# Optimization experiments

Hardware: AMD Instinct MI355X
Metric: run time of the kernel (lower is better)

The kernel has to match this reference:

```python
import jax, jax.numpy as jnp
import numpy as np

D_MODEL = 1024
N_HEADS = 16
D_K = 64


def setup_inputs() -> dict:
    key = jax.random.key(0)
    ks = jax.random.split(key, 9)
    dkh = D_K * N_HEADS
    s = 1.0 / np.sqrt(D_MODEL)
    so = 1.0 / np.sqrt(dkh)
    return {
        "x": jax.random.normal(ks[0], (2, 2048, D_MODEL), dtype=jnp.float32),
        "Wq": jax.random.normal(ks[1], (D_MODEL, dkh), dtype=jnp.float32) * s,
        "bq": jnp.zeros((dkh,), dtype=jnp.float32),
        "Wk": jax.random.normal(ks[2], (D_MODEL, dkh), dtype=jnp.float32) * s,
        "bk": jnp.zeros((dkh,), dtype=jnp.float32),
        "Wv": jax.random.normal(ks[3], (D_MODEL, dkh), dtype=jnp.float32) * s,
        "bv": jnp.zeros((dkh,), dtype=jnp.float32),
        "Wo": jax.random.normal(ks[4], (dkh, D_MODEL), dtype=jnp.float32) * so,
        "bo": jnp.zeros((D_MODEL,), dtype=jnp.float32),
    }


def reference(x, Wq, bq, Wk, bk, Wv, bv, Wo, bo):
    B, S, _ = x.shape
    # project and split heads: [B, S, H, Dk] -> [B, H, S, Dk]
    def split(t):
        return t.reshape(B, S, N_HEADS, D_K).transpose(0, 2, 1, 3)
    q = split(x @ Wq + bq)
    k = split(x @ Wk + bk)
    v = split(x @ Wv + bv)
    scores = jnp.einsum("bhsd,bhtd->bhst", q, k) / jnp.sqrt(jnp.float32(D_K))
    weights = jax.nn.softmax(scores, axis=-1)
    out = jnp.einsum("bhst,bhtd->bhsd", weights, v)  # [B, H, S, Dk]
    out = out.transpose(0, 2, 1, 3).reshape(B, S, N_HEADS * D_K)
    return out @ Wo + bo
```

## Files before the change

### kernel.cpp

```cpp
#include <hip/hip_runtime.h>

typedef unsigned short u16;
typedef unsigned int u32;
typedef short bf16x4 __attribute__((ext_vector_type(4)));
typedef short bf16x8 __attribute__((ext_vector_type(8)));
typedef float f32x4 __attribute__((ext_vector_type(4)));
typedef u32 u32x2 __attribute__((ext_vector_type(2)));
typedef u32 u32x4 __attribute__((ext_vector_type(4)));

#define DEVINL __device__ __forceinline__

DEVINL u16 f2bf(float f) {
    u32 u = __builtin_bit_cast(u32, f);
    u32 r = u + 0x7fffu + ((u >> 16) & 1u);
    return (u16)(r >> 16);
}

DEVINL u32 pack2(float a, float b) {
    return (u32)f2bf(a) | ((u32)f2bf(b) << 16);
}

__global__ __launch_bounds__(256) void cast_x_kernel(const float4* __restrict__ in,
                                                     u16* __restrict__ outp) {
    int i = blockIdx.x * 256 + threadIdx.x;
    float4 v = in[i];
    ushort4 o;
    o.x = f2bf(v.x); o.y = f2bf(v.y); o.z = f2bf(v.z); o.w = f2bf(v.w);
    *(ushort4*)&outp[(size_t)i * 4] = o;
}

__global__ __launch_bounds__(256) void transpose_cast(
    const float* __restrict__ W0, const float* __restrict__ W1,
    const float* __restrict__ W2, const float* __restrict__ W3,
    u16* __restrict__ T0, u16* __restrict__ T1,
    u16* __restrict__ T2, u16* __restrict__ T3) {
    __shared__ __align__(16) u16 lds[64 * 68];
    int bid = blockIdx.x;
    const float* W; u16* T;
    switch (bid >> 8) {
        case 0:  W = W0; T = T0; break;
        case 1:  W = W1; T = T1; break;
        case 2:  W = W2; T = T2; break;
        default: W = W3; T = T3; break;
    }
    int tile = bid & 255;
    int k0 = (tile >> 4) << 6;
    int n0 = (tile & 15) << 6;
    int t = threadIdx.x;
    int rk = t >> 2;
    int cb = (t & 3) << 4;
#pragma unroll
    for (int j = 0; j < 4; ++j) {
        float4 v = *(const float4*)&W[(size_t)(k0 + rk) * 1024 + n0 + cb + 4 * j];
        ushort4 o;
        o.x = f2bf(v.x); o.y = f2bf(v.y); o.z = f2bf(v.z); o.w = f2bf(v.w);
        *(ushort4*)&lds[rk * 68 + cb + 4 * j] = o;
    }
    __syncthreads();
    int rn = t >> 2;
#pragma unroll
    for (int j2 = 0; j2 < 2; ++j2) {
        u16 tmp[8];
#pragma unroll
        for (int u = 0; u < 8; ++u)
            tmp[u] = lds[(cb + 8 * j2 + u) * 68 + rn];
        *(uint4*)&T[(size_t)(n0 + rn) * 1024 + k0 + cb + 8 * j2] = *(uint4*)tmp;
    }
}

template <int MODE>
__global__ __launch_bounds__(256) void gemm_kernel(
    const u16* __restrict__ A,
    const u16* __restrict__ W0t, const u16* __restrict__ W1t, const u16* __restrict__ W2t,
    const float* __restrict__ b0, const float* __restrict__ b1, const float* __restrict__ b2,
    u16* __restrict__ Oq, u16* __restrict__ Ok, u16* __restrict__ Ov,
    float* __restrict__ Fout) {
    constexpr int NB = (MODE == 0) ? 24 : 8;
    const int mb = blockIdx.x / NB, nb = blockIdx.x % NB;
    const int m0 = mb * 128, n0 = nb * 128;
    const int tid = threadIdx.x, lane = tid & 63, w = tid >> 6;
    const int wr = w >> 1, wc = w & 1;
    const int c = lane & 15, g = lane >> 4;

    __shared__ __align__(16) u16 Alds[128 * 64];
    __shared__ __align__(16) u16 Blds[128 * 64];

    const u16* Wt; const float* bias; int ncol0;
    if (MODE == 0) {
        const int tsel = n0 >> 10;
        Wt   = (tsel == 0) ? W0t : ((tsel == 1) ? W1t : W2t);
        bias = (tsel == 0) ? b0  : ((tsel == 1) ? b1  : b2);
        ncol0 = n0 & 1023;
    } else {
        Wt = W0t; bias = b0; ncol0 = n0;
    }

    const u16* Asrc = A  + (size_t)(m0    + 32 * w + (lane >> 3)) * 1024 + (lane & 7) * 8;
    const u16* Bsrc = Wt + (size_t)(ncol0 + 32 * w + (lane >> 3)) * 1024 + (lane & 7) * 8;
    u16* AldsW = &Alds[(32 * w) * 64];
    u16* BldsW = &Blds[(32 * w) * 64];

    f32x4 acc[4][4] = {};

    for (int kt = 0; kt < 16; ++kt) {
        const int k0 = kt * 64;
#pragma unroll
        for (int i = 0; i < 4; ++i) {
            __builtin_amdgcn_global_load_lds(
                (const __attribute__((address_space(1))) void*)(Asrc + k0 + i * 8 * 1024),
                (__attribute__((address_space(3))) void*)(AldsW + i * 8 * 64), 16, 0, 0);
            __builtin_amdgcn_global_load_lds(
                (const __attribute__((address_space(1))) void*)(Bsrc + k0 + i * 8 * 1024),
                (__attribute__((address_space(3))) void*)(BldsW + i * 8 * 64), 16, 0, 0);
        }
        __syncthreads();
#pragma unroll
        for (int kk = 0; kk < 2; ++kk) {
            bf16x8 af[4], bfr[4];
#pragma unroll
            for (int mf = 0; mf < 4; ++mf)
                af[mf] = *(const bf16x8*)&Alds[(c + 16 * mf + 64 * wr) * 64 + 8 * g + 32 * kk];
#pragma unroll
            for (int nf = 0; nf < 4; ++nf)
                bfr[nf] = *(const bf16x8*)&Blds[(c + 16 * nf + 64 * wc) * 64 + 8 * g + 32 * kk];
#pragma unroll
            for (int mf = 0; mf < 4; ++mf)
#pragma unroll
                for (int nf = 0; nf < 4; ++nf)
                    acc[mf][nf] = __builtin_amdgcn_mfma_f32_16x16x32_bf16(
                        af[mf], bfr[nf], acc[mf][nf], 0, 0, 0);
        }
        __syncthreads();
    }

    float biasv[4];
#pragma unroll
    for (int nf = 0; nf < 4; ++nf) biasv[nf] = bias[ncol0 + 64 * wc + 16 * nf + c];

    if (MODE == 0) {
        const int bi = m0 >> 11;
        const int tsel = n0 >> 10;
        if (tsel < 2) {
            u16* Odst = (tsel == 0) ? Oq : Ok;
            const float sc = (tsel == 0) ? 0.125f : 1.0f;
#pragma unroll
            for (int nf = 0; nf < 4; ++nf) {
                const int n_in = ncol0 + 64 * wc + 16 * nf + c;
                const int h = n_in >> 6, d = n_in & 63;
                u16* base = Odst + ((size_t)(bi * 16 + h)) * 2048 * 64 + d;
#pragma unroll
                for (int mf = 0; mf < 4; ++mf)
#pragma unroll
                    for (int r = 0; r < 4; ++r) {
                        const int m = m0 + 64 * wr + 16 * mf + 4 * g + r;
                        const int s = m & 2047;
                        base[(size_t)s * 64] = f2bf((acc[mf][nf][r] + biasv[nf]) * sc);
                    }
            }
        } else {
#pragma unroll
            for (int nf = 0; nf < 4; ++nf) {
                const int n_in = ncol0 + 64 * wc + 16 * nf + c;
                const int h = n_in >> 6, d = n_in & 63;
                u16* base = Ov + ((size_t)((bi * 16 + h) * 64 + d)) * 2048;
#pragma unroll
                for (int mf = 0; mf < 4; ++mf) {
                    const int s = (m0 & 2047) + 64 * wr + 16 * mf + 4 * g;
                    u32x2 pr = {pack2(acc[mf][nf][0] + biasv[nf], acc[mf][nf][1] + biasv[nf]),
                                pack2(acc[mf][nf][2] + biasv[nf], acc[mf][nf][3] + biasv[nf])};
                    *(u32x2*)&base[s] = pr;
                }
            }
        }
    } else {
#pragma unroll
        for (int mf = 0; mf < 4; ++mf)
#pragma unroll
            for (int r = 0; r < 4; ++r) {
                const int m = m0 + 64 * wr + 16 * mf + 4 * g + r;
                float* rowp = Fout + (size_t)m * 1024 + n0 + 64 * wc;
#pragma unroll
                for (int nf = 0; nf < 4; ++nf)
                    rowp[16 * nf + c] = acc[mf][nf][r] + biasv[nf];
            }
    }
}

__global__ __launch_bounds__(256) void attn_kernel(
    const u16* __restrict__ Q, const u16* __restrict__ K, const u16* __restrict__ Vt,
    u16* __restrict__ O) {
    const int bid0 = blockIdx.x;
    const int bid = (bid0 & 7) * 128 + (bid0 >> 3);
    const int qb = bid & 31, h = (bid >> 5) & 15, b = bid >> 9;
    const int tid = threadIdx.x, lane = tid & 63, w = tid >> 6;
    const int c = lane & 15, g = lane >> 4;

    __shared__ __align__(16) u16 Klds[2][64 * 72];
    __shared__ __align__(16) u16 Vlds[2][64 * 72];

    const size_t hoff = ((size_t)(b * 16 + h)) * 2048 * 64;
    const u16* Qh = Q + hoff;
    const u16* Kh = K + hoff;
    const u16* Vh = Vt + hoff;

    const int q = qb * 64 + w * 16 + c;
    bf16x8 qf[2];
#pragma unroll
    for (int kk = 0; kk < 2; ++kk)
        qf[kk] = *(const bf16x8*)&Qh[(size_t)q * 64 + 8 * g + 32 * kk];

    f32x4 oacc[4] = {};
    float mrun = -3.0e38f, lrun = 0.f;

    const int srow = tid >> 3;
    const int scol = (tid & 7) * 8;

    {
        uint4 ka  = *(const uint4*)&Kh[(size_t)srow * 64 + scol];
        uint4 kb2 = *(const uint4*)&Kh[(size_t)(srow + 32) * 64 + scol];
        uint4 va  = *(const uint4*)&Vh[(size_t)srow * 2048 + scol];
        uint4 vb  = *(const uint4*)&Vh[(size_t)(srow + 32) * 2048 + scol];
        *(uint4*)&Klds[0][srow * 72 + scol] = ka;
        *(uint4*)&Klds[0][(srow + 32) * 72 + scol] = kb2;
        *(uint4*)&Vlds[0][srow * 72 + scol] = va;
        *(uint4*)&Vlds[0][(srow + 32) * 72 + scol] = vb;
    }
    __syncthreads();

    for (int kt = 0; kt < 32; ++kt) {
        const int cur = kt & 1, nxt = cur ^ 1;
        uint4 ka, kb2, va, vb;
        if (kt < 31) {
            ka  = *(const uint4*)&Kh[(size_t)((kt + 1) * 64 + srow) * 64 + scol];
            kb2 = *(const uint4*)&Kh[(size_t)((kt + 1) * 64 + srow + 32) * 64 + scol];
            va  = *(const uint4*)&Vh[(size_t)srow * 2048 + (kt + 1) * 64 + scol];
            vb  = *(const uint4*)&Vh[(size_t)(srow + 32) * 2048 + (kt + 1) * 64 + scol];
        }
        const u16* Kb0 = &Klds[cur][0];
        const u16* Vb0 = &Vlds[cur][0];

        f32x4 sacc[4] = {};
#pragma unroll
        for (int T = 0; T < 4; ++T)
#pragma unroll
            for (int kk = 0; kk < 2; ++kk) {
                bf16x8 kf = *(const bf16x8*)&Kb0[(16 * T + c) * 72 + 8 * g + 32 * kk];
                sacc[T] = __builtin_amdgcn_mfma_f32_16x16x32_bf16(kf, qf[kk], sacc[T], 0, 0, 0);
            }

        float t0 = fmaxf(fmaxf(sacc[0][0], sacc[0][1]), fmaxf(sacc[0][2], sacc[0][3]));
        float t1 = fmaxf(fmaxf(sacc[1][0], sacc[1][1]), fmaxf(sacc[1][2], sacc[1][3]));
        float t2 = fmaxf(fmaxf(sacc[2][0], sacc[2][1]), fmaxf(sacc[2][2], sacc[2][3]));
        float t3 = fmaxf(fmaxf(sacc[3][0], sacc[3][1]), fmaxf(sacc[3][2], sacc[3][3]));
        float mx = fmaxf(fmaxf(t0, t1), fmaxf(t2, t3));
        mx = fmaxf(mx, __shfl_xor(mx, 16));
        mx = fmaxf(mx, __shfl_xor(mx, 32));

        if (__any(mx > mrun)) {
            const float mnew = fmaxf(mrun, mx);
            const float alpha = __expf(mrun - mnew);
            mrun = mnew;
            lrun *= alpha;
#pragma unroll
            for (int dt = 0; dt < 4; ++dt)
#pragma unroll
                for (int r = 0; r < 4; ++r) oacc[dt][r] *= alpha;
        }

        u32 pw[4][2];
        float lsum = 0.f;
#pragma unroll
        for (int T = 0; T < 4; ++T) {
            float p0 = __expf(sacc[T][0] - mrun);
            float p1 = __expf(sacc[T][1] - mrun);
            float p2 = __expf(sacc[T][2] - mrun);
            float p3 = __expf(sacc[T][3] - mrun);
            lsum += (p0 + p1) + (p2 + p3);
            pw[T][0] = pack2(p0, p1);
            pw[T][1] = pack2(p2, p3);
        }
        lsum += __shfl_xor(lsum, 16);
        lsum += __shfl_xor(lsum, 32);
        lrun += lsum;

#pragma unroll
        for (int kb = 0; kb < 2; ++kb) {
            u32x4 ww = {pw[2 * kb][0], pw[2 * kb][1], pw[2 * kb + 1][0], pw[2 * kb + 1][1]};
            bf16x8 pf = __builtin_bit_cast(bf16x8, ww);
#pragma unroll
            for (int dt = 0; dt < 4; ++dt) {
                bf16x4 v0 = *(const bf16x4*)&Vb0[(16 * dt + c) * 72 + 32 * kb + 4 * g];
                bf16x4 v1 = *(const bf16x4*)&Vb0[(16 * dt + c) * 72 + 32 * kb + 16 + 4 * g];
                bf16x8 vf = __builtin_shufflevector(v0, v1, 0, 1, 2, 3, 4, 5, 6, 7);
                oacc[dt] = __builtin_amdgcn_mfma_f32_16x16x32_bf16(vf, pf, oacc[dt], 0, 0, 0);
            }
        }

        if (kt < 31) {
            *(uint4*)&Klds[nxt][srow * 72 + scol] = ka;
            *(uint4*)&Klds[nxt][(srow + 32) * 72 + scol] = kb2;
            *(uint4*)&Vlds[nxt][srow * 72 + scol] = va;
            *(uint4*)&Vlds[nxt][(srow + 32) * 72 + scol] = vb;
        }
        __syncthreads();
    }

    const float inv = 1.0f / lrun;
    const size_t obase = ((size_t)(b * 2048 + q)) * 1024 + h * 64 + 4 * g;
#pragma unroll
    for (int dt = 0; dt < 4; ++dt) {
        u32x2 pr = {pack2(oacc[dt][0] * inv, oacc[dt][1] * inv),
                    pack2(oacc[dt][2] * inv, oacc[dt][3] * inv)};
        *(u32x2*)&O[obase + 16 * dt] = pr;
    }
}

extern "C" void kernel_launch(void* const* d_in, const int* in_sizes, int n_in,
                              void* d_out, int out_size, void* d_ws, size_t ws_size,
                              hipStream_t stream) {
    const float* x  = (const float*)d_in[0];
    const float* Wq = (const float*)d_in[1];
    const float* bq = (const float*)d_in[2];
    const float* Wk = (const float*)d_in[3];
    const float* bk = (const float*)d_in[4];
    const float* Wv = (const float*)d_in[5];
    const float* bv = (const float*)d_in[6];
    const float* Wo = (const float*)d_in[7];
    const float* bo = (const float*)d_in[8];
    float* out = (float*)d_out;

    if (ws_size < (size_t)51 * 1024 * 1024) return;

    u16* ws  = (u16*)d_ws;
    u16* xb  = ws;
    u16* wqt = xb  + 4096 * 1024;
    u16* wkt = wqt + 1024 * 1024;
    u16* wvt = wkt + 1024 * 1024;
    u16* wot = wvt + 1024 * 1024;
    u16* Qb  = wot + 1024 * 1024;
    u16* Kb  = Qb + 4194304;
    u16* Vtb = Kb + 4194304;
    u16* Ob  = Vtb + 4194304;

    cast_x_kernel<<<4096, 256, 0, stream>>>((const float4*)x, xb);
    transpose_cast<<<1024, 256, 0, stream>>>(Wq, Wk, Wv, Wo, wqt, wkt, wvt, wot);
    gemm_kernel<0><<<768, 256, 0, stream>>>(xb, wqt, wkt, wvt, bq, bk, bv,
                                            Qb, Kb, Vtb, nullptr);
    attn_kernel<<<1024, 256, 0, stream>>>(Qb, Kb, Vtb, Ob);
    gemm_kernel<1><<<256, 256, 0, stream>>>(Ob, wot, nullptr, nullptr, bo, nullptr, nullptr,
                                            nullptr, nullptr, nullptr, out);
}
```

Baseline: 245.2 us.

## Drop LDS staging in attention; read K/V fragments directly from global memory

The attention kernel no longer stages K and V tiles through double-buffered LDS with per-iteration __syncthreads. Each lane now loads its MFMA operand fragments straight from global memory, relying on caches for reuse across the four waves. The V projection epilogue writes V^T in a permuted column order so each lane's 8-element PV fragment is one contiguous 16-byte load, and pack2 switches to the library bf16 conversion. This removes barriers and LDS traffic, but adds redundant global/L2 loads and leaves no explicit prefetch to hide load latency.

```diff
diff --git a/kernel.cpp b/kernel.cpp
--- a/kernel.cpp
+++ b/kernel.cpp
@@ -1,4 +1,5 @@
 #include <hip/hip_runtime.h>
+#include <hip/hip_bf16.h>
 
 typedef unsigned short u16;
 typedef unsigned int u32;
@@ -17,7 +18,9 @@
 }
 
 DEVINL u32 pack2(float a, float b) {
-    return (u32)f2bf(a) | ((u32)f2bf(b) << 16);
+    u16 lo = __builtin_bit_cast(u16, __float2bfloat16(a));
+    u16 hi = __builtin_bit_cast(u16, __float2bfloat16(b));
+    return (u32)lo | ((u32)hi << 16);
 }
 
 __global__ __launch_bounds__(256) void cast_x_kernel(const float4* __restrict__ in,
@@ -166,9 +169,12 @@
 #pragma unroll
                 for (int mf = 0; mf < 4; ++mf) {
                     const int s = (m0 & 2047) + 64 * wr + 16 * mf + 4 * g;
+                    const int r5 = s & 31;
+                    const int pos = (s & ~63) + 32 * ((s >> 5) & 1)
+                                  + ((r5 < 16) ? (2 * r5) : (2 * (r5 - 16) + 4));
                     u32x2 pr = {pack2(acc[mf][nf][0] + biasv[nf], acc[mf][nf][1] + biasv[nf]),
                                 pack2(acc[mf][nf][2] + biasv[nf], acc[mf][nf][3] + biasv[nf])};
-                    *(u32x2*)&base[s] = pr;
+                    *(u32x2*)&base[pos] = pr;
                 }
             }
         }
@@ -187,7 +193,7 @@
 }
 
 __global__ __launch_bounds__(256) void attn_kernel(
-    const u16* __restrict__ Q, const u16* __restrict__ K, const u16* __restrict__ Vt,
+    const u16* __restrict__ Q, const u16* __restrict__ K, const u16* __restrict__ Vp,
     u16* __restrict__ O) {
     const int bid0 = blockIdx.x;
     const int bid = (bid0 & 7) * 128 + (bid0 >> 3);
@@ -195,13 +201,10 @@
     const int tid = threadIdx.x, lane = tid & 63, w = tid >> 6;
     const int c = lane & 15, g = lane >> 4;
 
-    __shared__ __align__(16) u16 Klds[2][64 * 72];
-    __shared__ __align__(16) u16 Vlds[2][64 * 72];
-
     const size_t hoff = ((size_t)(b * 16 + h)) * 2048 * 64;
     const u16* Qh = Q + hoff;
     const u16* Kh = K + hoff;
-    const u16* Vh = Vt + hoff;
+    const u16* Vh = Vp + hoff;
 
     const int q = qb * 64 + w * 16 + c;
     bf16x8 qf[2];
@@ -209,42 +212,22 @@
     for (int kk = 0; kk < 2; ++kk)
         qf[kk] = *(const bf16x8*)&Qh[(size_t)q * 64 + 8 * g + 32 * kk];
 
+    const u16* pK = Kh + (size_t)c * 64 + 8 * g;
+    const u16* pV = Vh + (size_t)c * 2048 + 8 * g;
+
     f32x4 oacc[4] = {};
     float mrun = -3.0e38f, lrun = 0.f;
 
-    const int srow = tid >> 3;
-    const int scol = (tid & 7) * 8;
-
-    {
-        uint4 ka  = *(const uint4*)&Kh[(size_t)srow * 64 + scol];
-        uint4 kb2 = *(const uint4*)&Kh[(size_t)(srow + 32) * 64 + scol];
-        uint4 va  = *(const uint4*)&Vh[(size_t)srow * 2048 + scol];
-        uint4 vb  = *(const uint4*)&Vh[(size_t)(srow + 32) * 2048 + scol];
-        *(uint4*)&Klds[0][srow * 72 + scol] = ka;
-        *(uint4*)&Klds[0][(srow + 32) * 72 + scol] = kb2;
-        *(uint4*)&Vlds[0][srow * 72 + scol] = va;
-        *(uint4*)&Vlds[0][(srow + 32) * 72 + scol] = vb;
-    }
-    __syncthreads();
-
     for (int kt = 0; kt < 32; ++kt) {
-        const int cur = kt & 1, nxt = cur ^ 1;
-        uint4 ka, kb2, va, vb;
-        if (kt < 31) {
-            ka  = *(const uint4*)&Kh[(size_t)((kt + 1) * 64 + srow) * 64 + scol];
-            kb2 = *(const uint4*)&Kh[(size_t)((kt + 1) * 64 + srow + 32) * 64 + scol];
-            va  = *(const uint4*)&Vh[(size_t)srow * 2048 + (kt + 1) * 64 + scol];
-            vb  = *(const uint4*)&Vh[(size_t)(srow + 32) * 2048 + (kt + 1) * 64 + scol];
-        }
-        const u16* Kb0 = &Klds[cur][0];
-        const u16* Vb0 = &Vlds[cur][0];
+        const int koff = kt * 4096;
+        const int voff = kt * 64;
 
         f32x4 sacc[4] = {};
 #pragma unroll
         for (int T = 0; T < 4; ++T)
 #pragma unroll
             for (int kk = 0; kk < 2; ++kk) {
-                bf16x8 kf = *(const bf16x8*)&Kb0[(16 * T + c) * 72 + 8 * g + 32 * kk];
+                bf16x8 kf = *(const bf16x8*)&pK[koff + T * 1024 + 32 * kk];
                 sacc[T] = __builtin_amdgcn_mfma_f32_16x16x32_bf16(kf, qf[kk], sacc[T], 0, 0, 0);
             }
 
@@ -289,20 +272,10 @@
             bf16x8 pf = __builtin_bit_cast(bf16x8, ww);
 #pragma unroll
             for (int dt = 0; dt < 4; ++dt) {
-                bf16x4 v0 = *(const bf16x4*)&Vb0[(16 * dt + c) * 72 + 32 * kb + 4 * g];
-                bf16x4 v1 = *(const bf16x4*)&Vb0[(16 * dt + c) * 72 + 32 * kb + 16 + 4 * g];
-                bf16x8 vf = __builtin_shufflevector(v0, v1, 0, 1, 2, 3, 4, 5, 6, 7);
+                bf16x8 vf = *(const bf16x8*)&pV[voff + dt * 32768 + 32 * kb];
                 oacc[dt] = __builtin_amdgcn_mfma_f32_16x16x32_bf16(vf, pf, oacc[dt], 0, 0, 0);
             }
         }
-
-        if (kt < 31) {
-            *(uint4*)&Klds[nxt][srow * 72 + scol] = ka;
-            *(uint4*)&Klds[nxt][(srow + 32) * 72 + scol] = kb2;
-            *(uint4*)&Vlds[nxt][srow * 72 + scol] = va;
-            *(uint4*)&Vlds[nxt][(srow + 32) * 72 + scol] = vb;
-        }
-        __syncthreads();
     }
 
     const float inv = 1.0f / lrun;
```

Result: slower. 393.6 us (+60.5%).
